# Kernel tuning notes

Hardware: AMD Instinct MI355X
Metric: run time of the kernel (lower is better)

Reference implementation:

```python
import jax, jax.numpy as jnp
import numpy as np

B = 64        # graphs per batch
N_PER = 1024  # nodes per graph (equal-size graphs -> to_dense_batch mask is all-true)
C = 128       # in_channels
K = 64        # pooled clusters (k)
DEG = 32      # average degree
N = B * N_PER
E = N * DEG


def setup_inputs() -> dict:
    key = jax.random.key(0)
    k1, k2, k3, k4, k5 = jax.random.split(key, 5)
    x = jax.random.normal(k1, (N, C), dtype=jnp.float32)
    # edges constrained to stay within each graph (PyG batched-graph invariant)
    src_l = jax.random.randint(k2, (B, N_PER * DEG), 0, N_PER)
    dst_l = jax.random.randint(k3, (B, N_PER * DEG), 0, N_PER)
    off = (jnp.arange(B) * N_PER)[:, None]
    edge_index = jnp.stack([(src_l + off).reshape(-1), (dst_l + off).reshape(-1)], axis=0)
    batch = jnp.repeat(jnp.arange(B), N_PER)
    W_msg = jax.random.normal(k4, (C, K), dtype=jnp.float32) / np.float32(np.sqrt(C))
    W_root = jax.random.normal(k5, (C, K), dtype=jnp.float32) / np.float32(np.sqrt(C))
    b = jnp.zeros((K,), dtype=jnp.float32)
    return {"x": x, "edge_index": edge_index, "batch": batch,
            "W_msg": W_msg, "W_root": W_root, "b": b}


def reference(x, edge_index, batch, W_msg, W_root, b):
    src, dst = edge_index[0], edge_index[1]
    # ---- LSSMP: learned-score message passing -> cluster scores s [N, K] ----
    m = jax.nn.elu(x @ W_msg)                                  # per-node messages [N, K]
    agg = jax.ops.segment_sum(m[src], dst, num_segments=N)     # scatter-add over edges
    s = jnp.tanh(agg + x @ W_root + b)                         # act = tanh
    # ---- to_dense_batch (equal-size graphs: pure reshape, mask all-true) ----
    xd = x.reshape(B, N_PER, C)
    sd = s.reshape(B, N_PER, K)
    # ---- to_dense_adj ----
    g = src // N_PER
    adj = jnp.zeros((B, N_PER, N_PER), jnp.float32).at[g, src % N_PER, dst % N_PER].add(1.0)
    # ---- dense_connect: S = softmax(s); out = S^T X ; out_adj = S^T A S ----
    S = jax.nn.softmax(sd, axis=-1)                            # [B, N_PER, K]
    out = jnp.einsum('bnk,bnc->bkc', S, xd)                    # [B, K, C]
    out_adj = jnp.einsum('bkn,bnm,bml->bkl',
                         S.transpose(0, 2, 1), adj, S)         # [B, K, K]
    # ---- to_sparse_batch: pooled adjacency is dense -> all-pairs edges ----
    x_out = out.reshape(B * K, C)
    grid = jnp.stack(jnp.meshgrid(jnp.arange(K), jnp.arange(K), indexing='ij'), 0).reshape(2, -1)
    offs = (jnp.arange(B) * K)[None, :, None]
    edge_index_out = (grid[:, None, :] + offs).reshape(2, -1)  # [2, B*K*K]
    batch_out = jnp.repeat(jnp.arange(B), K)
    # original returns (x, edge_index, None, batch, None, None); adj values are dropped
    del out_adj
    return x_out, edge_index_out, batch_out
```

## Files before the change

### kernel.cpp

```cpp
#include <hip/hip_runtime.h>
#include <hip/hip_bf16.h>

typedef __hip_bfloat16 bf16;

#define NPER 1024
#define CC   128
#define KK   64
#define NTOT 65536
#define ETOT 2097152
#define EPG  32768
#define ESL  8192

#define M_OFF    0
#define R_OFF    8388608
#define SORT_OFF 16777216
#define RP_OFF   20971520
#define FLAG_OFF 21233664
#define ZB_OFF   21233728
#define WS_NEED  21233984ULL
#define WF_OFF   21233984
#define WS_NEED2 21266752ULL
#define GH_OFF   M_OFF
#define GC_OFF   (M_OFF + 2097152)

typedef short bf16x8 __attribute__((ext_vector_type(8)));
typedef float f32x4 __attribute__((ext_vector_type(4)));

__device__ __forceinline__ float t15_rb(float v) {
    return __bfloat162float(__float2bfloat16(v));
}
__device__ __forceinline__ float t15_bf(unsigned short h) {
    unsigned int w = ((unsigned int)h) << 16;
    float f;
    __builtin_memcpy(&f, &w, 4);
    return f;
}
__device__ __forceinline__ unsigned short t15_f2b(float f) {
    bf16 h = __float2bfloat16(f);
    unsigned short u;
    __builtin_memcpy(&u, &h, 2);
    return u;
}

__device__ __forceinline__ int t15_src(const int* ei, int e, int mode) {
    return (mode == 2 ? ei[2 * e] : ei[e]) & 65535;
}
__device__ __forceinline__ int t15_dst(const int* ei, int e, int mode) {
    return (mode == 2 ? ei[2 * ETOT + 2 * e] : ei[ETOT + e]) & 65535;
}

__global__ __launch_bounds__(1024) void t15_hist(const int* __restrict__ ei,
                                                 int* __restrict__ ghist) {
    __shared__ int hist[2048];
    __shared__ int sdet[1024];
    __shared__ int smode;
    int t = threadIdx.x;
    int blk = blockIdx.x;
    int ebase = blk * ESL;
    sdet[t] = ei[2 * (ebase + t) + 1];
    __syncthreads();
    for (int off = 512; off; off >>= 1) {
        if (t < off) sdet[t] |= sdet[t + off];
        __syncthreads();
    }
    if (t == 0) smode = (sdet[0] != 0) ? 1 : 2;
    hist[t] = 0;
    hist[t + 1024] = 0;
    __syncthreads();
    int mode = smode;
    for (int i = t; i < ESL; i += 1024) {
        int e = ebase + i;
        int s = t15_src(ei, e, mode) & (NPER - 1);
        int d = t15_dst(ei, e, mode) & (NPER - 1);
        atomicAdd(&hist[(d << 1) | ((s >> 9) & 1)], 1);
    }
    __syncthreads();
    ghist[blk * 2048 + t] = hist[t];
    ghist[blk * 2048 + 1024 + t] = hist[t + 1024];
}

__global__ __launch_bounds__(1024) void t15_scan(const int* __restrict__ ghist,
                                                 int* __restrict__ gcur,
                                                 unsigned short* __restrict__ rowptr,
                                                 float* __restrict__ zbias) {
    __shared__ int sh[8192];
    __shared__ int sscan[1024];
    int t = threadIdx.x, g = blockIdx.x;
    if (g == 0 && t < 64) zbias[t] = 0.f;
    for (int i = t; i < 8192; i += 1024) sh[i] = ghist[g * 8192 + i];
    __syncthreads();
    int b0 = 2 * t, b1 = 2 * t + 1;
    int h0[4], h1[4];
    int c0 = 0, c1 = 0;
#pragma unroll
    for (int q = 0; q < 4; ++q) {
        h0[q] = sh[q * 2048 + b0]; c0 += h0[q];
        h1[q] = sh[q * 2048 + b1]; c1 += h1[q];
    }
    int ts = c0 + c1;
    sscan[t] = ts;
    __syncthreads();
    for (int off = 1; off < 1024; off <<= 1) {
        int v = sscan[t];
        int a = (t >= off) ? sscan[t - off] : 0;
        __syncthreads();
        sscan[t] = v + a;
        __syncthreads();
    }
    int incl = sscan[t], excl = incl - ts;
    rowptr[g * 2048 + b0] = (unsigned short)(excl + c0);
    rowptr[g * 2048 + b1] = (unsigned short)incl;
    int r0 = excl, r1 = excl + c0;
#pragma unroll
    for (int q = 0; q < 4; ++q) {
        gcur[(g * 4 + q) * 2048 + b0] = r0; r0 += h0[q];
        gcur[(g * 4 + q) * 2048 + b1] = r1; r1 += h1[q];
    }
}

__global__ __launch_bounds__(1024) void t15_scat(const int* __restrict__ ei,
                                                 const int* __restrict__ gcur,
                                                 unsigned short* __restrict__ sorted) {
    __shared__ int cur[2048];
    __shared__ int sdet[1024];
    __shared__ int smode;
    int t = threadIdx.x, blk = blockIdx.x;
    int ebase = blk * ESL;
    int g = blk >> 2;
    sdet[t] = ei[2 * (ebase + t) + 1];
    __syncthreads();
    for (int off = 512; off; off >>= 1) {
        if (t < off) sdet[t] |= sdet[t + off];
        __syncthreads();
    }
    if (t == 0) smode = (sdet[0] != 0) ? 1 : 2;
    cur[t] = gcur[blk * 2048 + t];
    cur[t + 1024] = gcur[blk * 2048 + 1024 + t];
    __syncthreads();
    int mode = smode;
    unsigned short* sg = sorted + g * EPG;
    for (int i = t; i < ESL; i += 1024) {
        int e = ebase + i;
        int s = t15_src(ei, e, mode) & (NPER - 1);
        int d = t15_dst(ei, e, mode) & (NPER - 1);
        int pos = atomicAdd(&cur[(d << 1) | ((s >> 9) & 1)], 1);
        if ((unsigned)pos < (unsigned)EPG) sg[pos] = (unsigned short)s;
    }
}

__global__ void t15_wprep(const float* __restrict__ Wm, const float* __restrict__ Wr,
                          unsigned short* __restrict__ wf) {
    int t = threadIdx.x;
    for (int idx = t; idx < 16384; idx += 256) {
        int w = idx >> 13;
        int r = idx & 8191;
        int fr = r >> 3;
        int j = r & 7;
        int lane = fr & 63;
        int sc = fr >> 6;
        int step = sc >> 2, ct = sc & 3;
        int c = step * 32 + 8 * (lane >> 4) + j;
        int kk = ct * 16 + (lane & 15);
        const float* W = w ? Wr : Wm;
        wf[idx] = t15_f2b(W[c * 64 + kk]);
    }
}

__global__ __launch_bounds__(256) void t15_mroot_mfma(
        const float* __restrict__ x, const unsigned short* __restrict__ wf,
        const float* __restrict__ bias,
        bf16* __restrict__ m_out, bf16* __restrict__ root_out) {
    __shared__ unsigned short sX[64 * CC];
    int t = threadIdx.x;
    int lane = t & 63;
    int wv = t >> 6;
    int ww = wv & 1;
    int ct0 = (wv >> 1) * 2;
    int rl = lane & 15, g2 = lane >> 4;

    bf16x8 bq[4][2];
    const uint4* wfq = (const uint4*)wf;
#pragma unroll
    for (int step = 0; step < 4; ++step)
#pragma unroll
        for (int cti = 0; cti < 2; ++cti) {
            uint4 u = wfq[(size_t)(((ww * 4 + step) * 4) + ct0 + cti) * 64 + lane];
            bq[step][cti] = __builtin_bit_cast(bf16x8, u);
        }
    float bv0 = bias[ct0 * 16 + rl];
    float bv1 = bias[ct0 * 16 + 16 + rl];
    bf16* dst = ww ? root_out : m_out;

    for (int ti = 0; ti < 2; ++ti) {
        int tile = blockIdx.x * 2 + ti;
        size_t rowbase = (size_t)tile * 64;
        if (ti) __syncthreads();
        const float4* xg = (const float4*)(x + rowbase * CC);
        for (int i = t; i < 2048; i += 256) {
            float4 v = xg[i];
            int row = i >> 5;
            int cb = (i & 31) * 8;
            int addr = row * 256 + (cb ^ ((row & 7) << 4));
            ushort4 h;
            h.x = t15_f2b(v.x); h.y = t15_f2b(v.y);
            h.z = t15_f2b(v.z); h.w = t15_f2b(v.w);
            *(ushort4*)((char*)sX + addr) = h;
        }
        __syncthreads();

        for (int rt = 0; rt < 4; ++rt) {
            int row = rt * 16 + rl;
            bf16x8 af[4];
#pragma unroll
            for (int step = 0; step < 4; ++step) {
                int addr = row * 256 + ((g2 * 16 + step * 64) ^ ((row & 7) << 4));
                uint4 u = *(const uint4*)((const char*)sX + addr);
                af[step] = __builtin_bit_cast(bf16x8, u);
            }
            f32x4 acc0 = {0.f, 0.f, 0.f, 0.f};
            f32x4 acc1 = {0.f, 0.f, 0.f, 0.f};
#pragma unroll
            for (int step = 0; step < 4; ++step) {
                acc0 = __builtin_amdgcn_mfma_f32_16x16x32_bf16(af[step], bq[step][0], acc0, 0, 0, 0);
                acc1 = __builtin_amdgcn_mfma_f32_16x16x32_bf16(af[step], bq[step][1], acc1, 0, 0, 0);
            }
            int n0 = (int)rowbase + rt * 16 + g2 * 4;
#pragma unroll
            for (int cti = 0; cti < 2; ++cti) {
                f32x4 a = cti ? acc1 : acc0;
                float bv = cti ? bv1 : bv0;
                int kk = (ct0 + cti) * 16 + rl;
#pragma unroll
                for (int r = 0; r < 4; ++r) {
                    float v = a[r];
                    if (ww) v += bv;
                    else    v = v > 0.f ? v : expm1f(v);
                    dst[(size_t)(n0 + r) * KK + kk] = __float2bfloat16(v);
                }
            }
        }
    }
}

__global__ void t15_mroot(const float* __restrict__ x, const float* __restrict__ Wm,
                          const float* __restrict__ Wr, const float* __restrict__ bias,
                          bf16* __restrict__ m_out, bf16* __restrict__ root_out) {
    __shared__ bf16 sWm[CC * KK];
    __shared__ bf16 sWr[CC * KK];
    __shared__ bf16 sX[64 * CC];
    int t = threadIdx.x;
    int nb = blockIdx.x * 64;
    for (int i = t; i < CC * KK; i += 256) {
        sWm[i] = __float2bfloat16(Wm[i]);
        sWr[i] = __float2bfloat16(Wr[i]);
    }
    const float4* xg = (const float4*)(x + (size_t)nb * CC);
    for (int i = t; i < (64 * CC) / 4; i += 256) {
        float4 v = xg[i];
        sX[i * 4 + 0] = __float2bfloat16(v.x);
        sX[i * 4 + 1] = __float2bfloat16(v.y);
        sX[i * 4 + 2] = __float2bfloat16(v.z);
        sX[i * 4 + 3] = __float2bfloat16(v.w);
    }
    int k = t & 63, rg = t >> 6;
    float bv = bias[k];
    __syncthreads();
    float accm[16], accr[16];
#pragma unroll
    for (int r = 0; r < 16; ++r) { accm[r] = 0.f; accr[r] = 0.f; }
    for (int c = 0; c < CC; ++c) {
        float wm = __bfloat162float(sWm[c * KK + k]);
        float wr = __bfloat162float(sWr[c * KK + k]);
#pragma unroll
        for (int r = 0; r < 16; ++r) {
            float xv = __bfloat162float(sX[(rg + 4 * r) * CC + c]);
            accm[r] += xv * wm;
            accr[r] += xv * wr;
        }
    }
#pragma unroll
    for (int r = 0; r < 16; ++r) {
        int n = nb + rg + 4 * r;
        float mv = accm[r];
        mv = mv > 0.f ? mv : expm1f(mv);
        m_out[(size_t)n * KK + k] = __float2bfloat16(mv);
        root_out[(size_t)n * KK + k] = __float2bfloat16(accr[r] + bv);
    }
}

__global__ __launch_bounds__(512, 4) void t15_gatherlds(
        const unsigned short* __restrict__ rowptr,
        const unsigned short* __restrict__ sorted_src,
        const unsigned short* __restrict__ m_in,
        bf16* __restrict__ rootS) {
    __shared__ unsigned short sM[512 * KK];
    int lane = threadIdx.x & 63;
    int wv = threadIdx.x >> 6;
    int g = blockIdx.x >> 3;
    int nl0 = (blockIdx.x & 7) * 128 + wv * 16;
    int nbase = g * NPER + nl0;
    const unsigned short* rp = rowptr + g * 2048;
    const unsigned short* idx = sorted_src + g * EPG;
    int b0 = 2 * nl0;

    unsigned rpv = 0;
    if (lane <= 32 && (b0 + lane) > 0) rpv = (unsigned)rp[b0 + lane - 1];

    float acc[16];
#pragma unroll
    for (int nn = 0; nn < 16; ++nn)
        acc[nn] = t15_bf(((const unsigned short*)rootS)[(size_t)(nbase + nn) * KK + lane]);

#pragma unroll
    for (int h = 0; h < 2; ++h) {
        unsigned vi[16];
#pragma unroll
        for (int nn = 0; nn < 16; ++nn) {
            int bb = 2 * nn + h;
            int s = (int)__builtin_amdgcn_readlane(rpv, bb);
            int e = (int)__builtin_amdgcn_readlane(rpv, bb + 1);
            if (s > EPG) s = EPG;
            if (e < s) e = s;
            if (e > EPG) e = EPG;
            int w0 = s >> 1;
            int wc = ((e + 1) >> 1) - w0;
            if (wc > 64) wc = 64;
            unsigned v = 0;
            if (lane < wc) v = *(const unsigned*)(idx + 2 * (w0 + lane));
            vi[nn] = v;
        }
        if (h) __syncthreads();
        const uint4* mg = (const uint4*)(m_in + ((size_t)g * NPER + h * 512) * KK);
        uint4* ml = (uint4*)sM;
        for (int i = threadIdx.x; i < (512 * KK) / 8; i += 512) ml[i] = mg[i];
        __syncthreads();

#pragma unroll
        for (int nn = 0; nn < 16; ++nn) {
            int bb = 2 * nn + h;
            int s = (int)__builtin_amdgcn_readlane(rpv, bb);
            int e = (int)__builtin_amdgcn_readlane(rpv, bb + 1);
            if (s > EPG) s = EPG;
            if (e < s) e = s;
            if (e > EPG) e = EPG;
            int w0 = s >> 1;
            int wc = ((e + 1) >> 1) - w0;
            if (wc > 64) wc = 64;
            float a0 = acc[nn], a1 = 0.f;
            int i = s;
            if (i < e && (i & 1)) {
                unsigned w = __builtin_amdgcn_readlane(vi[nn], 0);
                a0 += t15_bf(sM[((w >> 16) & 511u) * KK + lane]);
                ++i;
            }
            int elim = 2 * (w0 + wc);
            if (elim > e) elim = e;
            for (; i + 2 <= elim; i += 2) {
                unsigned w = __builtin_amdgcn_readlane(vi[nn], (i >> 1) - w0);
                a0 += t15_bf(sM[(w & 511u) * KK + lane]);
                a1 += t15_bf(sM[((w >> 16) & 511u) * KK + lane]);
            }
            if (i < elim) {
                unsigned w = __builtin_amdgcn_readlane(vi[nn], (i >> 1) - w0);
                a0 += t15_bf(sM[(w & 511u) * KK + lane]);
                ++i;
            }
            for (; i < e; ++i) {
                unsigned sv = __builtin_amdgcn_readfirstlane((unsigned)idx[i]);
                a0 += t15_bf(sM[(sv & 511u) * KK + lane]);
            }
            acc[nn] = a0 + a1;
        }
    }

#pragma unroll
    for (int nn = 0; nn < 16; ++nn) {
        float sv = tanhf(acc[nn]);
        float mx = sv;
        for (int o = 32; o; o >>= 1) mx = fmaxf(mx, __shfl_xor(mx, o, 64));
        float ev = expf(sv - mx);
        float sm = ev;
        for (int o = 32; o; o >>= 1) sm += __shfl_xor(sm, o, 64);
        rootS[(size_t)(nbase + nn) * KK + lane] = __float2bfloat16(ev / sm);
    }
}

__global__ __launch_bounds__(512) void t15_pool(const float* __restrict__ x,
                                                const bf16* __restrict__ S_in,
                                                float* __restrict__ outp) {
    __shared__ float sXf[64 * 32];
    __shared__ float sSf[64 * 64];
    __shared__ float sRed[256 * 9];
    int tt = threadIdx.x;
    int half = tt >> 8;
    int t = tt & 255;
    int gb = blockIdx.x >> 2;
    int q = blockIdx.x & 3;
    int cq = q * 32;
    int k0 = (t & 15) * 4;
    int c0 = (t >> 4) * 2;
    float acc[4][2];
#pragma unroll
    for (int a = 0; a < 4; ++a) { acc[a][0] = 0.f; acc[a][1] = 0.f; }
    int jbeg = half * 32, jend = jbeg + 32;
    for (int tile = 0; tile < 16; ++tile) {
        int nb = gb * NPER + tile * 64;
        for (int i = tt; i < 64 * 32; i += 512) {
            int row = i >> 5, col = i & 31;
            sXf[i] = x[(size_t)(nb + row) * CC + cq + col];
        }
        const uint2* sg = (const uint2*)(S_in + (size_t)nb * KK);
        for (int i = tt; i < 1024; i += 512) {
            uint2 u = sg[i];
            int b = i * 4;
            sSf[b + 0] = t15_bf((unsigned short)(u.x & 0xffff));
            sSf[b + 1] = t15_bf((unsigned short)(u.x >> 16));
            sSf[b + 2] = t15_bf((unsigned short)(u.y & 0xffff));
            sSf[b + 3] = t15_bf((unsigned short)(u.y >> 16));
        }
        __syncthreads();
        for (int j = jbeg; j < jend; ++j) {
            float4 sv = *(const float4*)(sSf + j * 64 + k0);
            float2 xv = *(const float2*)(sXf + j * 32 + c0);
            acc[0][0] += sv.x * xv.x; acc[0][1] += sv.x * xv.y;
            acc[1][0] += sv.y * xv.x; acc[1][1] += sv.y * xv.y;
            acc[2][0] += sv.z * xv.x; acc[2][1] += sv.z * xv.y;
            acc[3][0] += sv.w * xv.x; acc[3][1] += sv.w * xv.y;
        }
        __syncthreads();
    }
    if (half == 1) {
        float* r = sRed + t * 9;
        r[0] = acc[0][0]; r[1] = acc[0][1];
        r[2] = acc[1][0]; r[3] = acc[1][1];
        r[4] = acc[2][0]; r[5] = acc[2][1];
        r[6] = acc[3][0]; r[7] = acc[3][1];
    }
    __syncthreads();
    if (half == 0) {
        const float* r = sRed + t * 9;
        acc[0][0] += r[0]; acc[0][1] += r[1];
        acc[1][0] += r[2]; acc[1][1] += r[3];
        acc[2][0] += r[4]; acc[2][1] += r[5];
        acc[3][0] += r[6]; acc[3][1] += r[7];
#pragma unroll
        for (int a = 0; a < 4; ++a) {
            outp[(size_t)(gb * KK + k0 + a) * CC + cq + c0 + 0] = t15_rb(acc[a][0]);
            outp[(size_t)(gb * KK + k0 + a) * CC + cq + c0 + 1] = t15_rb(acc[a][1]);
        }
    }
}

__global__ void t15_edgefill(float* __restrict__ outp) {
    int gid = blockIdx.x * 256 + threadIdx.x;
    if (gid >= 528384) return;
    float val;
    if (gid < 524288) {
        int r = gid >> 18;
        int rem = gid & 262143;
        int b = rem >> 12;
        int p = rem & 4095;
        int v = (r == 0) ? (p >> 6) : (p & 63);
        val = (float)(v + b * 64);
    } else {
        val = (float)((gid - 524288) >> 6);
    }
    outp[524288 + gid] = t15_rb(val);
}

extern "C" void kernel_launch(void* const* d_in, const int* in_sizes, int n_in,
                              void* d_out, int out_size, void* d_ws, size_t ws_size,
                              hipStream_t stream) {
    const float* x = nullptr; const int* ei = nullptr;
    const float* Wm = nullptr; const float* Wr = nullptr; const float* bias = nullptr;
    for (int i = 0; i < n_in; ++i) {
        int s = in_sizes[i];
        if (s == 8388608 && !x)       x  = (const float*)d_in[i];
        else if (s == 4194304 && !ei) ei = (const int*)d_in[i];
        else if (s == 8192) { if (!Wm) Wm = (const float*)d_in[i]; else if (!Wr) Wr = (const float*)d_in[i]; }
        else if (s == 64 && !bias)    bias = (const float*)d_in[i];
    }
    if (!x)  x  = (const float*)d_in[0];
    if (!ei) ei = (const int*)d_in[1];
    if (!Wm && n_in > 3) Wm = (const float*)d_in[3];
    if (!Wr && n_in > 4) Wr = (const float*)d_in[4];

    float* outp = (float*)d_out;
    bool out_ok = (out_size >= 1052672);
    bool ws_ok  = (ws_size >= WS_NEED) && x && ei && Wm && Wr;
    bool wf_ok  = (ws_size >= WS_NEED2);

    if (out_ok) {
        t15_edgefill<<<2064, 256, 0, stream>>>(outp);
    }
    if (out_ok && ws_ok) {
        char* ws = (char*)d_ws;
        bf16*           m_buf  = (bf16*)(ws + M_OFF);
        bf16*           rootS  = (bf16*)(ws + R_OFF);
        unsigned short* sorted = (unsigned short*)(ws + SORT_OFF);
        unsigned short* rowptr = (unsigned short*)(ws + RP_OFF);
        float*          zbias  = (float*)(ws + ZB_OFF);
        unsigned short* wf     = (unsigned short*)(ws + WF_OFF);
        int*            ghist  = (int*)(ws + GH_OFF);
        int*            gcur   = (int*)(ws + GC_OFF);
        const float* bz = bias ? bias : zbias;

        if (wf_ok) t15_wprep<<<1, 256, 0, stream>>>(Wm, Wr, wf);
        t15_hist<<<256, 1024, 0, stream>>>(ei, ghist);
        t15_scan<<<64, 1024, 0, stream>>>(ghist, gcur, rowptr, zbias);
        t15_scat<<<256, 1024, 0, stream>>>(ei, gcur, sorted);
        if (wf_ok)
            t15_mroot_mfma<<<512, 256, 0, stream>>>(x, wf, bz, m_buf, rootS);
        else
            t15_mroot<<<NTOT / 64, 256, 0, stream>>>(x, Wm, Wr, bz, m_buf, rootS);
        t15_gatherlds<<<512, 512, 0, stream>>>(rowptr, sorted,
                                               (const unsigned short*)m_buf, rootS);
        t15_pool<<<256, 512, 0, stream>>>(x, rootS, outp);
    }
}
```

Measured before the change: 237.2 us.

## Use f16 MFMA for pooling matmul and fold weight prep into hist kernel

Replaces the scalar FP32 S^T X pooling kernel with a wave-level f16 MFMA version. S and X tiles are staged into XOR-swizzled LDS as half precision. The standalone weight-repacking launch is removed and done by an extra block of the histogram kernel, which saves one kernel launch. Converting x and S to f16 adds rounding error, and x values could overflow the f16 range, though the output is rounded to bf16 anyway.

```diff
diff --git a/kernel.cpp b/kernel.cpp
--- a/kernel.cpp
+++ b/kernel.cpp
@@ -24,6 +24,7 @@
 #define GC_OFF   (M_OFF + 2097152)
 
 typedef short bf16x8 __attribute__((ext_vector_type(8)));
+typedef _Float16 half8 __attribute__((ext_vector_type(8)));
 typedef float f32x4 __attribute__((ext_vector_type(4)));
 
 __device__ __forceinline__ float t15_rb(float v) {
@@ -50,12 +51,32 @@
 }
 
 __global__ __launch_bounds__(1024) void t15_hist(const int* __restrict__ ei,
-                                                 int* __restrict__ ghist) {
+                                                 int* __restrict__ ghist,
+                                                 const float* __restrict__ Wm,
+                                                 const float* __restrict__ Wr,
+                                                 unsigned short* __restrict__ wf) {
+    int t = threadIdx.x;
+    int blk = blockIdx.x;
+    if (blk == 256) {
+        if (!wf) return;
+        for (int idx = t; idx < 16384; idx += 1024) {
+            int w = idx >> 13;
+            int r = idx & 8191;
+            int fr = r >> 3;
+            int j = r & 7;
+            int lane = fr & 63;
+            int sc = fr >> 6;
+            int step = sc >> 2, ct = sc & 3;
+            int c = step * 32 + 8 * (lane >> 4) + j;
+            int kk = ct * 16 + (lane & 15);
+            const float* W = w ? Wr : Wm;
+            wf[idx] = t15_f2b(W[c * 64 + kk]);
+        }
+        return;
+    }
     __shared__ int hist[2048];
     __shared__ int sdet[1024];
     __shared__ int smode;
-    int t = threadIdx.x;
-    int blk = blockIdx.x;
     int ebase = blk * ESL;
     sdet[t] = ei[2 * (ebase + t) + 1];
     __syncthreads();
@@ -145,24 +166,6 @@
         int d = t15_dst(ei, e, mode) & (NPER - 1);
         int pos = atomicAdd(&cur[(d << 1) | ((s >> 9) & 1)], 1);
         if ((unsigned)pos < (unsigned)EPG) sg[pos] = (unsigned short)s;
-    }
-}
-
-__global__ void t15_wprep(const float* __restrict__ Wm, const float* __restrict__ Wr,
-                          unsigned short* __restrict__ wf) {
-    int t = threadIdx.x;
-    for (int idx = t; idx < 16384; idx += 256) {
-        int w = idx >> 13;
-        int r = idx & 8191;
-        int fr = r >> 3;
-        int j = r & 7;
-        int lane = fr & 63;
-        int sc = fr >> 6;
-        int step = sc >> 2, ct = sc & 3;
-        int c = step * 32 + 8 * (lane >> 4) + j;
-        int kk = ct * 16 + (lane & 15);
-        const float* W = w ? Wr : Wm;
-        wf[idx] = t15_f2b(W[c * 64 + kk]);
     }
 }
 
@@ -385,69 +388,73 @@
     }
 }
 
-__global__ __launch_bounds__(512) void t15_pool(const float* __restrict__ x,
-                                                const bf16* __restrict__ S_in,
-                                                float* __restrict__ outp) {
-    __shared__ float sXf[64 * 32];
-    __shared__ float sSf[64 * 64];
-    __shared__ float sRed[256 * 9];
+__global__ __launch_bounds__(512) void t15_pool_mfma(
+        const float* __restrict__ x, const bf16* __restrict__ S_in,
+        float* __restrict__ outp) {
+    __shared__ char sP[24576];
     int tt = threadIdx.x;
-    int half = tt >> 8;
-    int t = tt & 255;
-    int gb = blockIdx.x >> 2;
-    int q = blockIdx.x & 3;
-    int cq = q * 32;
-    int k0 = (t & 15) * 4;
-    int c0 = (t >> 4) * 2;
-    float acc[4][2];
-#pragma unroll
-    for (int a = 0; a < 4; ++a) { acc[a][0] = 0.f; acc[a][1] = 0.f; }
-    int jbeg = half * 32, jend = jbeg + 32;
-    for (int tile = 0; tile < 16; ++tile) {
-        int nb = gb * NPER + tile * 64;
-        for (int i = tt; i < 64 * 32; i += 512) {
-            int row = i >> 5, col = i & 31;
-            sXf[i] = x[(size_t)(nb + row) * CC + cq + col];
-        }
-        const uint2* sg = (const uint2*)(S_in + (size_t)nb * KK);
-        for (int i = tt; i < 1024; i += 512) {
-            uint2 u = sg[i];
-            int b = i * 4;
-            sSf[b + 0] = t15_bf((unsigned short)(u.x & 0xffff));
-            sSf[b + 1] = t15_bf((unsigned short)(u.x >> 16));
-            sSf[b + 2] = t15_bf((unsigned short)(u.y & 0xffff));
-            sSf[b + 3] = t15_bf((unsigned short)(u.y >> 16));
-        }
-        __syncthreads();
-        for (int j = jbeg; j < jend; ++j) {
-            float4 sv = *(const float4*)(sSf + j * 64 + k0);
-            float2 xv = *(const float2*)(sXf + j * 32 + c0);
-            acc[0][0] += sv.x * xv.x; acc[0][1] += sv.x * xv.y;
-            acc[1][0] += sv.y * xv.x; acc[1][1] += sv.y * xv.y;
-            acc[2][0] += sv.z * xv.x; acc[2][1] += sv.z * xv.y;
-            acc[3][0] += sv.w * xv.x; acc[3][1] += sv.w * xv.y;
-        }
-        __syncthreads();
-    }
-    if (half == 1) {
-        float* r = sRed + t * 9;
-        r[0] = acc[0][0]; r[1] = acc[0][1];
-        r[2] = acc[1][0]; r[3] = acc[1][1];
-        r[4] = acc[2][0]; r[5] = acc[2][1];
-        r[6] = acc[3][0]; r[7] = acc[3][1];
-    }
-    __syncthreads();
-    if (half == 0) {
-        const float* r = sRed + t * 9;
-        acc[0][0] += r[0]; acc[0][1] += r[1];
-        acc[1][0] += r[2]; acc[1][1] += r[3];
-        acc[2][0] += r[4]; acc[2][1] += r[5];
-        acc[3][0] += r[6]; acc[3][1] += r[7];
-#pragma unroll
-        for (int a = 0; a < 4; ++a) {
-            outp[(size_t)(gb * KK + k0 + a) * CC + cq + c0 + 0] = t15_rb(acc[a][0]);
-            outp[(size_t)(gb * KK + k0 + a) * CC + cq + c0 + 1] = t15_rb(acc[a][1]);
-        }
+    int lane = tt & 63;
+    int wv = tt >> 6;
+    int mt = wv & 3;
+    int nt = wv >> 2;
+    int rl = lane & 15, g2 = lane >> 4;
+    int g = blockIdx.x >> 2;
+    int cq = (blockIdx.x & 3) * 32;
+
+    f32x4 acc = {0.f, 0.f, 0.f, 0.f};
+
+    for (int tile = 0; tile < 8; ++tile) {
+        size_t nbase = (size_t)g * NPER + tile * 128;
+        if (tile) __syncthreads();
+        const uint2* sg = (const uint2*)(S_in + nbase * KK);
+        for (int i = 0; i < 4; ++i) {
+            int idx = tt + 512 * i;
+            int r = idx >> 4;
+            int q = idx & 15;
+            uint2 u = sg[idx];
+            unsigned short b[4] = {(unsigned short)(u.x & 0xffff),
+                                   (unsigned short)(u.x >> 16),
+                                   (unsigned short)(u.y & 0xffff),
+                                   (unsigned short)(u.y >> 16)};
+#pragma unroll
+            for (int j = 0; j < 4; ++j) {
+                int k = 4 * q + j;
+                _Float16 h = (_Float16)t15_bf(b[j]);
+                *(_Float16*)(sP + k * 256 + ((2 * r) ^ ((k & 7) << 4))) = h;
+            }
+        }
+        const float* xb = x + nbase * CC + cq;
+        for (int i = 0; i < 2; ++i) {
+            int idx = tt + 512 * i;
+            int r = idx >> 3;
+            int q = idx & 7;
+            float4 v = *(const float4*)(xb + (size_t)r * CC + 4 * q);
+#pragma unroll
+            for (int j = 0; j < 4; ++j) {
+                int c = 4 * q + j;
+                float fv = (j == 0) ? v.x : (j == 1) ? v.y : (j == 2) ? v.z : v.w;
+                _Float16 h = (_Float16)fv;
+                *(_Float16*)(sP + 16384 + c * 256 + ((2 * r) ^ ((c & 7) << 4))) = h;
+            }
+        }
+        __syncthreads();
+#pragma unroll
+        for (int ks = 0; ks < 4; ++ks) {
+            int nb2 = 2 * (32 * ks + 8 * g2);
+            int arow = 16 * mt + rl;
+            uint4 ua = *(const uint4*)(sP + arow * 256 + (nb2 ^ ((arow & 7) << 4)));
+            int brow = 16 * nt + rl;
+            uint4 ub = *(const uint4*)(sP + 16384 + brow * 256 + (nb2 ^ ((brow & 7) << 4)));
+            half8 A = __builtin_bit_cast(half8, ua);
+            half8 B = __builtin_bit_cast(half8, ub);
+            acc = __builtin_amdgcn_mfma_f32_16x16x32_f16(A, B, acc, 0, 0, 0);
+        }
+    }
+
+#pragma unroll
+    for (int r = 0; r < 4; ++r) {
+        int krow = 16 * mt + 4 * g2 + r;
+        outp[(size_t)(g * KK + krow) * CC + cq + 16 * nt + rl] = t15_rb(acc[r]);
     }
 }
 
@@ -500,13 +507,12 @@
         unsigned short* sorted = (unsigned short*)(ws + SORT_OFF);
         unsigned short* rowptr = (unsigned short*)(ws + RP_OFF);
         float*          zbias  = (float*)(ws + ZB_OFF);
-        unsigned short* wf     = (unsigned short*)(ws + WF_OFF);
+        unsigned short* wf     = wf_ok ? (unsigned short*)(ws + WF_OFF) : nullptr;
         int*            ghist  = (int*)(ws + GH_OFF);
         int*            gcur   = (int*)(ws + GC_OFF);
         const float* bz = bias ? bias : zbias;
 
-        if (wf_ok) t15_wprep<<<1, 256, 0, stream>>>(Wm, Wr, wf);
-        t15_hist<<<256, 1024, 0, stream>>>(ei, ghist);
+        t15_hist<<<257, 1024, 0, stream>>>(ei, ghist, Wm, Wr, wf);
         t15_scan<<<64, 1024, 0, stream>>>(ghist, gcur, rowptr, zbias);
         t15_scat<<<256, 1024, 0, stream>>>(ei, gcur, sorted);
         if (wf_ok)
@@ -515,6 +521,6 @@
             t15_mroot<<<NTOT / 64, 256, 0, stream>>>(x, Wm, Wr, bz, m_buf, rootS);
         t15_gatherlds<<<512, 512, 0, stream>>>(rowptr, sorted,
                                                (const unsigned short*)m_buf, rootS);
-        t15_pool<<<256, 512, 0, stream>>>(x, rootS, outp);
-    }
-}
+        t15_pool_mfma<<<256, 512, 0, stream>>>(x, rootS, outp);
+    }
+}
```

After: 202.2 us. 1.17x faster.
